# Optimization experiments

Hardware: AMD Instinct MI355X
Metric: run time of the kernel (lower is better)

## Reference

```python
import jax, jax.numpy as jnp
import numpy as np

N_NODES, N_EDGES, D_IN, N_GRAPHS = 20000, 320000, 256, 32
H1, C1, H2, C2 = 4, 128, 4, 64


def setup_inputs() -> dict:
    key = jax.random.key(0)
    ks = jax.random.split(key, 24)
    g = lambda k, shape, fan: jax.random.normal(k, shape, jnp.float32) * (1.0 / np.sqrt(fan))
    inp = {
        'x': jax.random.normal(ks[0], (N_NODES, D_IN), jnp.float32),
        'edge_index': jax.random.randint(ks[1], (2, N_EDGES), 0, N_NODES, jnp.int32),
        'batch': jnp.sort(jax.random.randint(ks[2], (N_NODES,), 0, N_GRAPHS, jnp.int32)),
        'edge_attr': jax.random.normal(ks[3], (N_EDGES, 1), jnp.float32),
        # GATConv 1: lin [D_IN, H1*C1], att_src/dst/edge [H1,C1], lin_edge [1,H1*C1], bias [H1*C1]
        'W1': g(ks[4], (D_IN, H1 * C1), D_IN),
        'as1': g(ks[5], (H1, C1), C1),
        'ad1': g(ks[6], (H1, C1), C1),
        'We1': g(ks[7], (1, H1 * C1), 1),
        'ae1': g(ks[8], (H1, C1), C1),
        'b1': jnp.zeros((H1 * C1,), jnp.float32),
        'g1': jnp.ones((H1 * C1,), jnp.float32),
        'be1': jnp.zeros((H1 * C1,), jnp.float32),
        # GATConv 2 (concat=False -> out 64)
        'W2': g(ks[9], (H1 * C1, H2 * C2), H1 * C1),
        'as2': g(ks[10], (H2, C2), C2),
        'ad2': g(ks[11], (H2, C2), C2),
        'We2': g(ks[12], (1, H2 * C2), 1),
        'ae2': g(ks[13], (H2, C2), C2),
        'b2': jnp.zeros((C2,), jnp.float32),
        'g2': jnp.ones((C2,), jnp.float32),
        'be2': jnp.zeros((C2,), jnp.float32),
        'fw1': g(ks[14], (C2, 32), C2),
        'fb1': jnp.zeros((32,), jnp.float32),
        'fw2': g(ks[15], (32, 1), 32),
        'fb2': jnp.zeros((1,), jnp.float32),
    }
    return inp


def _gat(x, src, dst, ea, W, a_s, a_d, We, a_e, bias, H, C, concat, n):
    h = (x @ W).reshape(n, H, C)                         # [N,H,C]
    al_s = jnp.einsum('nhc,hc->nh', h, a_s)              # [N,H]
    al_d = jnp.einsum('nhc,hc->nh', h, a_d)
    e = (ea @ We).reshape(-1, H, C)                      # [E',H,C]
    al_e = jnp.einsum('ehc,hc->eh', e, a_e)
    logits = jax.nn.leaky_relu(al_s[src] + al_d[dst] + al_e, 0.2)  # [E',H]
    m = jax.ops.segment_max(logits, dst, num_segments=n)
    m = jnp.where(jnp.isfinite(m), m, 0.0)
    p = jnp.exp(logits - m[dst])
    denom = jax.ops.segment_sum(p, dst, num_segments=n)
    alpha = p / (denom[dst] + 1e-16)                     # segment softmax
    out = jax.ops.segment_sum(h[src] * alpha[:, :, None], dst, num_segments=n)
    out = out.reshape(n, H * C) if concat else out.mean(axis=1)
    return out + bias


def _bn(x, gamma, beta):
    mu = x.mean(axis=0)
    var = x.var(axis=0)
    return gamma * (x - mu) * jax.lax.rsqrt(var + 1e-5) + beta


def reference(x, edge_index, batch, edge_attr, W1, as1, ad1, We1, ae1, b1, g1, be1,
              W2, as2, ad2, We2, ae2, b2, g2, be2, fw1, fb1, fw2, fb2):
    n = x.shape[0]
    loop = jnp.arange(n, dtype=edge_index.dtype)
    src = jnp.concatenate([edge_index[0], loop])
    dst = jnp.concatenate([edge_index[1], loop])
    # self-loop edge_attr filled with mean (PyG fill_value='mean')
    ea = jnp.concatenate([edge_attr, jnp.broadcast_to(edge_attr.mean(axis=0), (n, edge_attr.shape[1]))])

    h = _gat(x, src, dst, ea, W1, as1, ad1, We1, ae1, b1, H1, C1, True, n)
    h = jax.nn.elu(_bn(h, g1, be1))
    h = _gat(h, src, dst, ea, W2, as2, ad2, We2, ae2, b2, H2, C2, False, n)
    h = jax.nn.elu(_bn(h, g2, be2))

    sums = jax.ops.segment_sum(h, batch, num_segments=N_GRAPHS)
    cnt = jax.ops.segment_sum(jnp.ones((n,), h.dtype), batch, num_segments=N_GRAPHS)
    pooled = sums / jnp.maximum(cnt, 1.0)[:, None]       # global_mean_pool
    # dropout is identity in eval mode
    out = jax.nn.elu(pooled @ fw1 + fb1) @ fw2 + fb2
    return out
```

## Files before the change

### kernel.cpp

```cpp
#include <hip/hip_runtime.h>
#include <hip/hip_bf16.h>

#define N_NODES  20000
#define MPAD     20096
#define N_EDGES  320000
#define N_EP     (N_EDGES + N_NODES)
#define D_IN     256
#define N_GRAPHS 32
#define HH1 4
#define CC1 128
#define HH2 4
#define CC2 64
#define MAXDEG   128

#define XB_OFF      0ull
#define HB1_OFF     10289152ull
#define AGG1_OFF    30867456ull
#define HB2_OFF     51445760ull
#define OUT2_OFF    61734912ull
#define EAF_OFF     66854912ull
#define W1BT_OFF    68134912ull
#define W2BT_OFF    68397056ull
#define CSR_OFF     68659200ull
#define ROWPTR_OFF  71379200ull
#define GSTART_OFF  71459264ull
#define SMALL_OFF   71459520ull
#define SBUF_OFF    71485120ull
#define EAP_OFF     71485184ull
#define ALSP_OFF    71486464ull
#define ALDP_OFF    72129536ull
#define PMU1_OFF    72772608ull
#define PM21_OFF    73296896ull
#define PMU2_OFF    73821184ull
#define PM22_OFF    73886720ull
#define A1_OFF      73952256ull
#define B1_OFF      73954304ull
#define A2_OFF      73956352ull
#define B2_OFF      73956608ull
#define EAACC_OFF   73956864ull
#define ALS_OFF     73956928ull
#define ALD_OFF     74278464ull
#define DEG_OFF     74600000ull
#define CURS_OFF    74680000ull
#define FLAGZ_OFF   74760000ull
#define ZERO0_START DEG_OFF
#define ZERO0_SIZE  160128ull
#define PP_OFF      74760128ull

#define S_AS1 0
#define S_AD1 512
#define S_WE1 1024
#define S_AE1 1536
#define S_G1  2048
#define S_BE1 2560
#define S_AS2 3072
#define S_AD2 3328
#define S_WE2 3584
#define S_AE2 3840
#define S_G2  4096
#define S_BE2 4160
#define S_FW1 4224
#define S_FB1 6272
#define S_FW2 6304
#define S_FB2 6336

typedef __attribute__((ext_vector_type(8))) short bf8_t;
typedef __attribute__((ext_vector_type(4))) float f4_t;

__global__ void detect_dtype(const unsigned short* __restrict__ xr, int* __restrict__ flag) {
    int i = blockIdx.x * blockDim.x + threadIdx.x;
    unsigned short u = xr[i];
    if ((u & 0x7F80) == 0x7F80) atomicOr(flag, 1);
}

__device__ __forceinline__ float loadF(const void* p, int i, int fp32) {
    return fp32 ? ((const float*)p)[i]
                : __bfloat162float(((const __hip_bfloat16*)p)[i]);
}

#define PB_XB  5024
#define PB_EAF 313
#define PB_W   512
#define PB_SM  16
#define PREP_BLOCKS (PB_XB + PB_EAF + 2 * PB_W + PB_SM + 1)
__global__ __launch_bounds__(256) void prep(
        const int* __restrict__ flag,
        const void* x, const void* ea, const void* W1, const void* W2,
        const void* as1, const void* ad1, const void* We1, const void* ae1,
        const void* g1, const void* be1, const void* as2, const void* ad2,
        const void* We2, const void* ae2, const void* g2, const void* be2,
        const void* fw1, const void* fb1, const void* fw2, const void* fb2,
        __hip_bfloat16* __restrict__ xb, float* __restrict__ eaf, float* __restrict__ eap,
        __hip_bfloat16* __restrict__ W1bt, __hip_bfloat16* __restrict__ W2bt,
        float* __restrict__ smalls, float* __restrict__ sbuf) {
    __shared__ float sh[256];
    int b = blockIdx.x, t = threadIdx.x;
    int fp32 = flag[0];
    if (b < PB_XB) {
        int base = (b * 256 + t) * 4;
        __hip_bfloat16 tmp[4];
#pragma unroll
        for (int j = 0; j < 4; ++j) {
            int i = base + j;
            float v = (i < N_NODES * D_IN) ? loadF(x, i, fp32) : 0.f;
            tmp[j] = __float2bfloat16(v);
        }
        *(uint2*)&xb[base] = *(uint2*)tmp;
        return;
    }
    b -= PB_XB;
    if (b < PB_EAF) {
        int base = (b * 256 + t) * 4;
        float s = 0.f;
#pragma unroll
        for (int j = 0; j < 4; ++j) {
            int i = base + j;
            if (i < N_EDGES) { float v = loadF(ea, i, fp32); eaf[i] = v; s += v; }
        }
        sh[t] = s;
        __syncthreads();
        for (int st = 128; st; st >>= 1) {
            if (t < st) sh[t] += sh[t + st];
            __syncthreads();
        }
        if (t == 0) eap[b] = sh[0];
        return;
    }
    b -= PB_EAF;
    if (b < PB_W) {
        int i = b * 256 + t;
        int k = i >> 9, n = i & 511;
        W1bt[(size_t)n * 256 + k] = __float2bfloat16(loadF(W1, i, fp32));
        return;
    }
    b -= PB_W;
    if (b < PB_W) {
        int i = b * 256 + t;
        int k = i >> 8, n = i & 255;
        W2bt[(size_t)n * 512 + k] = __float2bfloat16(loadF(W2, i, fp32));
        return;
    }
    b -= PB_W;
    if (b < PB_SM) {
        const void* srcs[16] = {as1, ad1, We1, ae1, g1, be1, as2, ad2, We2, ae2, g2, be2, fw1, fb1, fw2, fb2};
        const int cnts[16] = {512, 512, 512, 512, 512, 512, 256, 256, 256, 256, 64, 64, 2048, 32, 32, 1};
        const int offs[16] = {S_AS1, S_AD1, S_WE1, S_AE1, S_G1, S_BE1, S_AS2, S_AD2,
                              S_WE2, S_AE2, S_G2, S_BE2, S_FW1, S_FB1, S_FW2, S_FB2};
        for (int i = t; i < cnts[b]; i += 256)
            smalls[offs[b] + i] = loadF(srcs[b], i, fp32);
        return;
    }
    if (t < 4) {
        float s = 0.f;
        for (int c = 0; c < CC1; ++c) s += loadF(We1, t * CC1 + c, fp32) * loadF(ae1, t * CC1 + c, fp32);
        sbuf[t] = s;
    } else if (t < 8) {
        int h = t - 4;
        float s = 0.f;
        for (int c = 0; c < CC2; ++c) s += loadF(We2, h * CC2 + c, fp32) * loadF(ae2, h * CC2 + c, fp32);
        sbuf[4 + h] = s;
    }
}

#define HIST_BLOCKS 1329
__global__ void hist_bounds(const int* __restrict__ ei, int* __restrict__ deg,
                            const int* __restrict__ batch, int* __restrict__ gstart) {
    int b = blockIdx.x, t = threadIdx.x;
    if (b < HIST_BLOCKS) {
        int e = b * 256 + t;
        if (e >= N_EP) return;
        int d = (e < N_EDGES) ? ei[N_EDGES + e] : e - N_EDGES;
        atomicAdd(&deg[d], 1);
        return;
    }
    int i = (b - HIST_BLOCKS) * 256 + t;
    if (i >= N_NODES) return;
    int bb = batch[i];
    if (i == 0) {
        for (int g = 0; g <= bb; ++g) gstart[g] = 0;
    } else {
        int pb = batch[i - 1];
        for (int g = pb + 1; g <= bb; ++g) gstart[g] = i;
    }
    if (i == N_NODES - 1) {
        for (int g = bb + 1; g <= N_GRAPHS; ++g) gstart[g] = N_NODES;
    }
}

__global__ __launch_bounds__(1024) void deg_scan(const int* __restrict__ deg, int* __restrict__ rowptr,
                                                 const float* __restrict__ eap, float* __restrict__ ea_acc) {
    __shared__ int part[1024];
    int t = threadIdx.x;
    int lo = t * 20;
    int hi = lo + 20; if (hi > N_NODES) hi = N_NODES; if (lo > N_NODES) lo = N_NODES;
    int s = 0;
    for (int i = lo; i < hi; ++i) s += deg[i];
    part[t] = s;
    __syncthreads();
    for (int off = 1; off < 1024; off <<= 1) {
        int u = (t >= off) ? part[t - off] : 0;
        __syncthreads();
        if (t >= off) part[t] += u;
        __syncthreads();
    }
    int run = part[t] - s;
    for (int i = lo; i < hi; ++i) { rowptr[i] = run; run += deg[i]; }
    if (hi == N_NODES && lo < N_NODES) rowptr[N_NODES] = run;
    if (t == 0) {
        float es = 0.f;
        for (int i = 0; i < PB_EAF; ++i) es += eap[i];
        ea_acc[0] = es;
    }
}

__global__ void edge_scatter(const int* __restrict__ ei, const int* __restrict__ rowptr,
                             int* __restrict__ cursor, int2* __restrict__ csr_se) {
    int e = blockIdx.x * blockDim.x + threadIdx.x;
    if (e >= N_EP) return;
    int s, d;
    if (e < N_EDGES) { s = ei[e]; d = ei[N_EDGES + e]; }
    else { s = d = e - N_EDGES; }
    int pos = rowptr[d] + atomicAdd(&cursor[d], 1);
    csr_se[pos] = make_int2(s, e);
}

__global__ __launch_bounds__(64) void csr_sort_fill(const int* __restrict__ rowptr, int2* __restrict__ cs,
                                                    const float* __restrict__ eaf,
                                                    const float* __restrict__ ea_acc) {
    __shared__ int2 buf[128];
    int d = blockIdx.x;
    int beg = rowptr[d], end = rowptr[d + 1], n = end - beg;
    int lane = threadIdx.x;
    float ea_mean = ea_acc[0] * (1.0f / N_EDGES);
    if (n <= 0) return;
    if (n <= 128) {
        for (int i = lane; i < n; i += 64) buf[i] = cs[beg + i];
        __syncthreads();
        for (int r = 0; r < n; ++r) {
            int i = 2 * lane + (r & 1);
            if (i + 1 < n) {
                int2 a = buf[i], b = buf[i + 1];
                if (a.y > b.y) { buf[i] = b; buf[i + 1] = a; }
            }
            __syncthreads();
        }
        for (int i = lane; i < n; i += 64) {
            int2 se = buf[i];
            float eav = (se.y < N_EDGES) ? eaf[se.y] : ea_mean;
            se.y = __float_as_int(eav);
            cs[beg + i] = se;
        }
    } else {
        if (lane == 0) {
            for (int i = beg + 1; i < end; ++i) {
                int2 key = cs[i]; int j = i - 1;
                while (j >= beg && cs[j].y > key.y) { cs[j + 1] = cs[j]; --j; }
                cs[j + 1] = key;
            }
        }
        __syncthreads();
        for (int i = lane; i < n; i += 64) {
            int2 se = cs[beg + i];
            float eav = (se.y < N_EDGES) ? eaf[se.y] : ea_mean;
            se.y = __float_as_int(eav);
            cs[beg + i] = se;
        }
    }
}

__global__ __launch_bounds__(256) void gemm_mfma_al(
        const short* __restrict__ A, const short* __restrict__ Bt,
        __hip_bfloat16* __restrict__ Cb, int N, int K,
        float* __restrict__ alsp, float* __restrict__ aldp,
        const float* __restrict__ asv, const float* __restrict__ adv, int cshift) {
    __shared__ short As[128 * 40];
    __shared__ short Bs[64 * 40];
    int t = threadIdx.x;
    int wv = t >> 6, lane = t & 63, quad = lane >> 4, lr = lane & 15;
    int m0 = blockIdx.y * 128, n0 = blockIdx.x * 64;
    f4_t acc[2][4] = {};
    int ra0 = t >> 2, sa0 = t & 3;
    int ra1 = (t + 256) >> 2;
    for (int k0 = 0; k0 < K; k0 += 32) {
        *(uint4*)&As[ra0 * 40 + sa0 * 8] = *(const uint4*)&A[(size_t)(m0 + ra0) * K + k0 + sa0 * 8];
        *(uint4*)&As[ra1 * 40 + sa0 * 8] = *(const uint4*)&A[(size_t)(m0 + ra1) * K + k0 + sa0 * 8];
        *(uint4*)&Bs[ra0 * 40 + sa0 * 8] = *(const uint4*)&Bt[(size_t)(n0 + ra0) * K + k0 + sa0 * 8];
        __syncthreads();
        bf8_t a0 = *(const bf8_t*)&As[(wv * 16 + lr) * 40 + quad * 8];
        bf8_t a1 = *(const bf8_t*)&As[((wv + 4) * 16 + lr) * 40 + quad * 8];
#pragma unroll
        for (int nt = 0; nt < 4; ++nt) {
            bf8_t b = *(const bf8_t*)&Bs[(nt * 16 + lr) * 40 + quad * 8];
            acc[0][nt] = __builtin_amdgcn_mfma_f32_16x16x32_bf16(a0, b, acc[0][nt], 0, 0, 0);
            acc[1][nt] = __builtin_amdgcn_mfma_f32_16x16x32_bf16(a1, b, acc[1][nt], 0, 0, 0);
        }
        __syncthreads();
    }
#pragma unroll
    for (int si = 0; si < 2; ++si) {
        int mrow = m0 + (wv + si * 4) * 16 + quad * 4;
#pragma unroll
        for (int nt = 0; nt < 4; ++nt) {
            int col = n0 + nt * 16 + lr;
#pragma unroll
            for (int r = 0; r < 4; ++r)
                Cb[(size_t)(mrow + r) * N + col] = __float2bfloat16(acc[si][nt][r]);
        }
    }
    float asv4[4], adv4[4];
#pragma unroll
    for (int nt = 0; nt < 4; ++nt) {
        asv4[nt] = asv[n0 + nt * 16 + lr];
        adv4[nt] = adv[n0 + nt * 16 + lr];
    }
    int hsel = n0 >> cshift;
    int parity = (n0 >> 6) & ((1 << (cshift - 6)) - 1);
#pragma unroll
    for (int si = 0; si < 2; ++si) {
#pragma unroll
        for (int r = 0; r < 4; ++r) {
            float ps = 0.f, pd = 0.f;
#pragma unroll
            for (int nt = 0; nt < 4; ++nt) {
                ps += acc[si][nt][r] * asv4[nt];
                pd += acc[si][nt][r] * adv4[nt];
            }
#pragma unroll
            for (int m = 1; m < 16; m <<= 1) {
                ps += __shfl_xor(ps, m);
                pd += __shfl_xor(pd, m);
            }
            if (lr == 0) {
                int row = m0 + (wv + si * 4) * 16 + quad * 4 + r;
                alsp[(row * 4 + hsel) * 2 + parity] = ps;
                aldp[(row * 4 + hsel) * 2 + parity] = pd;
            }
        }
    }
}

__global__ void al_combine(const float* __restrict__ alsp, const float* __restrict__ aldp,
                           float* __restrict__ als, float* __restrict__ ald, int nparts) {
    int i = blockIdx.x * blockDim.x + threadIdx.x;
    if (i >= MPAD * 4) return;
    float s = alsp[2 * i], d0 = aldp[2 * i];
    if (nparts == 2) { s += alsp[2 * i + 1]; d0 += aldp[2 * i + 1]; }
    als[i] = s; ald[i] = d0;
}

__global__ __launch_bounds__(128) void fused_agg1(
        const int* __restrict__ rowptr, const int2* __restrict__ cs,
        const float* __restrict__ als, const float* __restrict__ ald,
        const float* __restrict__ sbuf, const __hip_bfloat16* __restrict__ hb,
        __hip_bfloat16* __restrict__ outb) {
    __shared__ float lg[MAXDEG * 4];
    __shared__ int   ssrc[MAXDEG];
    __shared__ float red[4 * 128];
    __shared__ float mxs[4], dns[4];
    int d = blockIdx.x, t = threadIdx.x;
    int beg = rowptr[d], end = rowptr[d + 1], n = end - beg;
    bool fit = (n <= MAXDEG);
    float4 adv = *(const float4*)&ald[d * 4];
    float adh[4] = {adv.x, adv.y, adv.z, adv.w};
    float sb[4] = {sbuf[0], sbuf[1], sbuf[2], sbuf[3]};
    float mx[4] = {-INFINITY, -INFINITY, -INFINITY, -INFINITY};
    for (int p = t; p < n; p += 128) {
        int2 se = cs[beg + p];
        float eav = __int_as_float(se.y);
        float4 as = *(const float4*)&als[se.x * 4];
        float as4[4] = {as.x, as.y, as.z, as.w};
#pragma unroll
        for (int h = 0; h < 4; ++h) {
            float l = as4[h] + adh[h] + eav * sb[h];
            l = l > 0.f ? l : 0.2f * l;
            if (fit) lg[p * 4 + h] = l;
            mx[h] = fmaxf(mx[h], l);
        }
        if (fit) ssrc[p] = se.x;
    }
#pragma unroll
    for (int i = 0; i < 4; ++i) red[i * 128 + t] = mx[i];
    __syncthreads();
    for (int s = 64; s; s >>= 1) {
        if (t < s) {
#pragma unroll
            for (int i = 0; i < 4; ++i)
                red[i * 128 + t] = fmaxf(red[i * 128 + t], red[i * 128 + t + s]);
        }
        __syncthreads();
    }
    if (t < 4) mxs[t] = red[t * 128];
    __syncthreads();
    float m4[4] = {mxs[0], mxs[1], mxs[2], mxs[3]};
    float sm[4] = {0.f, 0.f, 0.f, 0.f};
    if (fit) {
        for (int p = t; p < n; p += 128) {
            float4 lv = *(float4*)&lg[p * 4];
            lv.x = __expf(lv.x - m4[0]); lv.y = __expf(lv.y - m4[1]);
            lv.z = __expf(lv.z - m4[2]); lv.w = __expf(lv.w - m4[3]);
            *(float4*)&lg[p * 4] = lv;
            sm[0] += lv.x; sm[1] += lv.y; sm[2] += lv.z; sm[3] += lv.w;
        }
    } else {
        for (int p = t; p < n; p += 128) {
            int2 se = cs[beg + p];
            float eav = __int_as_float(se.y);
            float4 as = *(const float4*)&als[se.x * 4];
            float as4[4] = {as.x, as.y, as.z, as.w};
#pragma unroll
            for (int h = 0; h < 4; ++h) {
                float l = as4[h] + adh[h] + eav * sb[h];
                l = l > 0.f ? l : 0.2f * l;
                sm[h] += __expf(l - m4[h]);
            }
        }
    }
    __syncthreads();
#pragma unroll
    for (int i = 0; i < 4; ++i) red[i * 128 + t] = sm[i];
    __syncthreads();
    for (int s = 64; s; s >>= 1) {
        if (t < s) {
#pragma unroll
            for (int i = 0; i < 4; ++i)
                red[i * 128 + t] += red[i * 128 + t + s];
        }
        __syncthreads();
    }
    if (t < 4) dns[t] = red[t * 128];
    __syncthreads();
    int h = t >> 5;
    float rdn = 1.0f / (dns[h] + 1e-16f);
    float a0 = 0.f, a1 = 0.f, a2 = 0.f, a3 = 0.f;
    if (fit) {
        for (int p = 0; p < n; ++p) {
            float w = lg[p * 4 + h];
            uint2 raw = *(const uint2*)&hb[(size_t)ssrc[p] * 512 + 4 * t];
            a0 += w * __uint_as_float(raw.x << 16);
            a1 += w * __uint_as_float(raw.x & 0xFFFF0000u);
            a2 += w * __uint_as_float(raw.y << 16);
            a3 += w * __uint_as_float(raw.y & 0xFFFF0000u);
        }
    } else {
        for (int p = 0; p < n; ++p) {
            int2 se = cs[beg + p];
            float eav = __int_as_float(se.y);
            float l = als[se.x * 4 + h] + adh[h] + eav * sb[h];
            l = l > 0.f ? l : 0.2f * l;
            float w = __expf(l - m4[h]);
            uint2 raw = *(const uint2*)&hb[(size_t)se.x * 512 + 4 * t];
            a0 += w * __uint_as_float(raw.x << 16);
            a1 += w * __uint_as_float(raw.x & 0xFFFF0000u);
            a2 += w * __uint_as_float(raw.y << 16);
            a3 += w * __uint_as_float(raw.y & 0xFFFF0000u);
        }
    }
    __hip_bfloat16 tmp[4] = {__float2bfloat16(a0 * rdn), __float2bfloat16(a1 * rdn),
                             __float2bfloat16(a2 * rdn), __float2bfloat16(a3 * rdn)};
    *(uint2*)&outb[(size_t)d * 512 + 4 * t] = *(uint2*)tmp;
}

__global__ __launch_bounds__(64) void fused_agg2(
        const int* __restrict__ rowptr, const int2* __restrict__ cs,
        const float* __restrict__ als, const float* __restrict__ ald,
        const float* __restrict__ sbuf, const __hip_bfloat16* __restrict__ hb,
        float* __restrict__ out2) {
    __shared__ float lg[MAXDEG * 4];
    __shared__ int   ssrc[MAXDEG];
    __shared__ float red[4 * 64];
    __shared__ float mxs[4], dns[4];
    __shared__ float shm[256];
    int d = blockIdx.x, t = threadIdx.x;
    int beg = rowptr[d], end = rowptr[d + 1], n = end - beg;
    bool fit = (n <= MAXDEG);
    float4 adv = *(const float4*)&ald[d * 4];
    float adh[4] = {adv.x, adv.y, adv.z, adv.w};
    float sb[4] = {sbuf[4], sbuf[5], sbuf[6], sbuf[7]};
    float mx[4] = {-INFINITY, -INFINITY, -INFINITY, -INFINITY};
    for (int p = t; p < n; p += 64) {
        int2 se = cs[beg + p];
        float eav = __int_as_float(se.y);
        float4 as = *(const float4*)&als[se.x * 4];
        float as4[4] = {as.x, as.y, as.z, as.w};
#pragma unroll
        for (int h = 0; h < 4; ++h) {
            float l = as4[h] + adh[h] + eav * sb[h];
            l = l > 0.f ? l : 0.2f * l;
            if (fit) lg[p * 4 + h] = l;
            mx[h] = fmaxf(mx[h], l);
        }
        if (fit) ssrc[p] = se.x;
    }
#pragma unroll
    for (int i = 0; i < 4; ++i) red[i * 64 + t] = mx[i];
    __syncthreads();
    for (int s = 32; s; s >>= 1) {
        if (t < s) {
#pragma unroll
            for (int i = 0; i < 4; ++i)
                red[i * 64 + t] = fmaxf(red[i * 64 + t], red[i * 64 + t + s]);
        }
        __syncthreads();
    }
    if (t < 4) mxs[t] = red[t * 64];
    __syncthreads();
    float m4[4] = {mxs[0], mxs[1], mxs[2], mxs[3]};
    float sm[4] = {0.f, 0.f, 0.f, 0.f};
    if (fit) {
        for (int p = t; p < n; p += 64) {
            float4 lv = *(float4*)&lg[p * 4];
            lv.x = __expf(lv.x - m4[0]); lv.y = __expf(lv.y - m4[1]);
            lv.z = __expf(lv.z - m4[2]); lv.w = __expf(lv.w - m4[3]);
            *(float4*)&lg[p * 4] = lv;
            sm[0] += lv.x; sm[1] += lv.y; sm[2] += lv.z; sm[3] += lv.w;
        }
    } else {
        for (int p = t; p < n; p += 64) {
            int2 se = cs[beg + p];
            float eav = __int_as_float(se.y);
            float4 as = *(const float4*)&als[se.x * 4];
            float as4[4] = {as.x, as.y, as.z, as.w};
#pragma unroll
            for (int h = 0; h < 4; ++h) {
                float l = as4[h] + adh[h] + eav * sb[h];
                l = l > 0.f ? l : 0.2f * l;
                sm[h] += __expf(l - m4[h]);
            }
        }
    }
    __syncthreads();
#pragma unroll
    for (int i = 0; i < 4; ++i) red[i * 64 + t] = sm[i];
    __syncthreads();
    for (int s = 32; s; s >>= 1) {
        if (t < s) {
#pragma unroll
            for (int i = 0; i < 4; ++i)
                red[i * 64 + t] += red[i * 64 + t + s];
        }
        __syncthreads();
    }
    if (t < 4) dns[t] = red[t * 64];
    __syncthreads();
    int h = t >> 4;
    float rdn = 1.0f / (dns[h] + 1e-16f);
    float a0 = 0.f, a1 = 0.f, a2 = 0.f, a3 = 0.f;
    if (fit) {
        for (int p = 0; p < n; ++p) {
            float w = lg[p * 4 + h];
            uint2 raw = *(const uint2*)&hb[(size_t)ssrc[p] * 256 + 4 * t];
            a0 += w * __uint_as_float(raw.x << 16);
            a1 += w * __uint_as_float(raw.x & 0xFFFF0000u);
            a2 += w * __uint_as_float(raw.y << 16);
            a3 += w * __uint_as_float(raw.y & 0xFFFF0000u);
        }
    } else {
        for (int p = 0; p < n; ++p) {
            int2 se = cs[beg + p];
            float eav = __int_as_float(se.y);
            float l = als[se.x * 4 + h] + adh[h] + eav * sb[h];
            l = l > 0.f ? l : 0.2f * l;
            float w = __expf(l - m4[h]);
            uint2 raw = *(const uint2*)&hb[(size_t)se.x * 256 + 4 * t];
            a0 += w * __uint_as_float(raw.x << 16);
            a1 += w * __uint_as_float(raw.x & 0xFFFF0000u);
            a2 += w * __uint_as_float(raw.y << 16);
            a3 += w * __uint_as_float(raw.y & 0xFFFF0000u);
        }
    }
    shm[4 * t] = a0 * rdn; shm[4 * t + 1] = a1 * rdn;
    shm[4 * t + 2] = a2 * rdn; shm[4 * t + 3] = a3 * rdn;
    __syncthreads();
    if (t < 16) {
        float4 v;
        v.x = 0.25f * (shm[4 * t] + shm[64 + 4 * t] + shm[128 + 4 * t] + shm[192 + 4 * t]);
        v.y = 0.25f * (shm[4 * t + 1] + shm[64 + 4 * t + 1] + shm[128 + 4 * t + 1] + shm[192 + 4 * t + 1]);
        v.z = 0.25f * (shm[4 * t + 2] + shm[64 + 4 * t + 2] + shm[128 + 4 * t + 2] + shm[192 + 4 * t + 2]);
        v.w = 0.25f * (shm[4 * t + 3] + shm[64 + 4 * t + 3] + shm[128 + 4 * t + 3] + shm[192 + 4 * t + 3]);
        *(float4*)&out2[(size_t)d * 64 + 4 * t] = v;
    }
}

__global__ __launch_bounds__(256) void bn_part_b(const __hip_bfloat16* __restrict__ x,
                                                 float* __restrict__ pmu, float* __restrict__ pm2) {
    int t = threadIdx.x, b = blockIdx.x;
    float s0 = 0.f, s20 = 0.f, s1 = 0.f, s21 = 0.f;
    for (int i = b; i < N_NODES; i += gridDim.x) {
        unsigned u = *(const unsigned*)&x[(size_t)i * 512 + 2 * t];
        float v0 = __uint_as_float(u << 16);
        float v1 = __uint_as_float(u & 0xFFFF0000u);
        s0 += v0; s20 += v0 * v0; s1 += v1; s21 += v1 * v1;
    }
    pmu[b * 512 + 2 * t] = s0;     pm2[b * 512 + 2 * t] = s20;
    pmu[b * 512 + 2 * t + 1] = s1; pm2[b * 512 + 2 * t + 1] = s21;
}

__global__ void bn_reduce_affine(const float* __restrict__ pmu, const float* __restrict__ pm2,
                                 const float* __restrict__ smalls, int s_g, int s_be,
                                 float* __restrict__ a, float* __restrict__ b, int nch) {
    int c = blockIdx.x * blockDim.x + threadIdx.x;
    if (c >= nch) return;
    float s = 0.f, s2 = 0.f;
    for (int bk = 0; bk < 256; ++bk) { s += pmu[bk * nch + c]; s2 += pm2[bk * nch + c]; }
    float m = s * (1.0f / N_NODES);
    float var = s2 * (1.0f / N_NODES) - m * m;
    float aa = smalls[s_g + c] * rsqrtf(var + 1e-5f);
    a[c] = aa;
    b[c] = smalls[s_be + c] - m * aa;
}

__global__ __launch_bounds__(256) void bn_apply_elu_b16(__hip_bfloat16* __restrict__ x,
                                                        const float* __restrict__ a,
                                                        const float* __restrict__ b) {
    int q = blockIdx.x * blockDim.x + threadIdx.x;
    if (q >= N_NODES * 512 / 4) return;
    int base = q * 4;
    int j = base & 511;
    uint2 raw = *(uint2*)&x[base];
    float v[4] = {__uint_as_float(raw.x << 16), __uint_as_float(raw.x & 0xFFFF0000u),
                  __uint_as_float(raw.y << 16), __uint_as_float(raw.y & 0xFFFF0000u)};
    __hip_bfloat16 tmp[4];
#pragma unroll
    for (int k = 0; k < 4; ++k) {
        float y = a[j + k] * v[k] + b[j + k];
        y = y > 0.f ? y : expm1f(y);
        tmp[k] = __float2bfloat16(y);
    }
    *(uint2*)&x[base] = *(uint2*)tmp;
}

__global__ __launch_bounds__(256) void bn2_stats(const float* __restrict__ x,
                                                 float* __restrict__ pmu, float* __restrict__ pm2) {
    int t = threadIdx.x;
    int c = t & 63, j = t >> 6;
    float ls = 0.f, ls2 = 0.f;
    for (int nd = blockIdx.x * 4 + j; nd < N_NODES; nd += gridDim.x * 4) {
        float v = x[(size_t)nd * 64 + c];
        ls += v; ls2 += v * v;
    }
    __shared__ float shs[4][64], sh2[4][64];
    shs[j][c] = ls; sh2[j][c] = ls2;
    __syncthreads();
    if (j == 0) {
        pmu[blockIdx.x * 64 + c] = shs[0][c] + shs[1][c] + shs[2][c] + shs[3][c];
        pm2[blockIdx.x * 64 + c] = sh2[0][c] + sh2[1][c] + sh2[2][c] + sh2[3][c];
    }
}

__global__ __launch_bounds__(256) void pool_part(const float* __restrict__ x, const int* __restrict__ gstart,
                                                 const float* __restrict__ a2, const float* __restrict__ b2,
                                                 float* __restrict__ pp) {
    int g = blockIdx.x >> 3, ck = blockIdx.x & 7;
    int t = threadIdx.x;
    int c = t & 63, j = t >> 6;
    int beg = gstart[g], end = gstart[g + 1], n = end - beg;
    int cb = beg + (n * ck) / 8, ce = beg + (n * (ck + 1)) / 8;
    float ac = a2[c], bc = b2[c];
    float s = 0.f;
    for (int i = cb + j; i < ce; i += 4) {
        float y = ac * x[(size_t)i * 64 + c] + bc;
        s += (y > 0.f ? y : expm1f(y));
    }
    __shared__ float sh[4][64];
    sh[j][c] = s;
    __syncthreads();
    if (j == 0)
        pp[blockIdx.x * 64 + c] = sh[0][c] + sh[1][c] + sh[2][c] + sh[3][c];
}

__global__ __launch_bounds__(64) void pool_mlp_fin(const float* __restrict__ pp, const int* __restrict__ gstart,
                                                   const float* __restrict__ smalls, const int* __restrict__ flag,
                                                   void* __restrict__ outp) {
    int g = blockIdx.x, t = threadIdx.x;
    __shared__ float pooled[64];
    __shared__ float hsh[32];
    float s = 0.f;
    for (int k = 0; k < 8; ++k) s += pp[(g * 8 + k) * 64 + t];
    int n = gstart[g + 1] - gstart[g];
    pooled[t] = s / fmaxf((float)n, 1.0f);
    __syncthreads();
    if (t < 32) {
        float acc = smalls[S_FB1 + t];
        for (int cc = 0; cc < 64; ++cc)
            acc += pooled[cc] * smalls[S_FW1 + cc * 32 + t];
        hsh[t] = acc > 0.f ? acc : expm1f(acc);
    }
    __syncthreads();
    if (t == 0) {
        float o = smalls[S_FB2];
        for (int k = 0; k < 32; ++k) o += hsh[k] * smalls[S_FW2 + k];
        if (flag[0]) ((float*)outp)[g] = o;
        else ((__hip_bfloat16*)outp)[g] = __float2bfloat16(o);
    }
}

extern "C" void kernel_launch(void* const* d_in, const int* in_sizes, int n_in,
                              void* d_out, int out_size, void* d_ws, size_t ws_size,
                              hipStream_t stream) {
    const void* x    = d_in[0];
    const int* ei    = (const int*)d_in[1];
    const int* batch = (const int*)d_in[2];
    const void* ea   = d_in[3];
    const void* W1   = d_in[4];
    const void* as1  = d_in[5];
    const void* ad1  = d_in[6];
    const void* We1  = d_in[7];
    const void* ae1  = d_in[8];
    const void* g1   = d_in[10];
    const void* be1  = d_in[11];
    const void* W2   = d_in[12];
    const void* as2  = d_in[13];
    const void* ad2  = d_in[14];
    const void* We2  = d_in[15];
    const void* ae2  = d_in[16];
    const void* g2   = d_in[18];
    const void* be2  = d_in[19];
    const void* fw1  = d_in[20];
    const void* fb1  = d_in[21];
    const void* fw2  = d_in[22];
    const void* fb2  = d_in[23];

    char* ws = (char*)d_ws;
    __hip_bfloat16* xb   = (__hip_bfloat16*)(ws + XB_OFF);
    __hip_bfloat16* hb1  = (__hip_bfloat16*)(ws + HB1_OFF);
    __hip_bfloat16* agg1 = (__hip_bfloat16*)(ws + AGG1_OFF);
    __hip_bfloat16* hb2  = (__hip_bfloat16*)(ws + HB2_OFF);
    float* out2   = (float*)(ws + OUT2_OFF);
    float* eaf    = (float*)(ws + EAF_OFF);
    __hip_bfloat16* W1bt = (__hip_bfloat16*)(ws + W1BT_OFF);
    __hip_bfloat16* W2bt = (__hip_bfloat16*)(ws + W2BT_OFF);
    int2*  csr_se = (int2*)(ws + CSR_OFF);
    int*   rowptr = (int*)(ws + ROWPTR_OFF);
    int*   gstart = (int*)(ws + GSTART_OFF);
    float* smalls = (float*)(ws + SMALL_OFF);
    float* sbuf   = (float*)(ws + SBUF_OFF);
    float* eap    = (float*)(ws + EAP_OFF);
    float* alsp   = (float*)(ws + ALSP_OFF);
    float* aldp   = (float*)(ws + ALDP_OFF);
    float* pmu1   = (float*)(ws + PMU1_OFF);
    float* pm21   = (float*)(ws + PM21_OFF);
    float* pmu2   = (float*)(ws + PMU2_OFF);
    float* pm22   = (float*)(ws + PM22_OFF);
    float* a1     = (float*)(ws + A1_OFF);
    float* b1     = (float*)(ws + B1_OFF);
    float* a2     = (float*)(ws + A2_OFF);
    float* b2     = (float*)(ws + B2_OFF);
    float* ea_acc = (float*)(ws + EAACC_OFF);
    float* als    = (float*)(ws + ALS_OFF);
    float* ald    = (float*)(ws + ALD_OFF);
    float* pp     = (float*)(ws + PP_OFF);
    int*   deg    = (int*)(ws + DEG_OFF);
    int*   cursor = (int*)(ws + CURS_OFF);
    int*   flag   = (int*)(ws + FLAGZ_OFF);

    hipMemsetAsync(ws + ZERO0_START, 0, ZERO0_SIZE, stream);

    detect_dtype<<<256, 256, 0, stream>>>((const unsigned short*)x, flag);
    prep<<<PREP_BLOCKS, 256, 0, stream>>>(flag, x, ea, W1, W2,
                                          as1, ad1, We1, ae1, g1, be1, as2, ad2,
                                          We2, ae2, g2, be2, fw1, fb1, fw2, fb2,
                                          xb, eaf, eap, W1bt, W2bt, smalls, sbuf);

    hist_bounds<<<HIST_BLOCKS + 79, 256, 0, stream>>>(ei, deg, batch, gstart);
    deg_scan<<<1, 1024, 0, stream>>>(deg, rowptr, eap, ea_acc);
    edge_scatter<<<HIST_BLOCKS, 256, 0, stream>>>(ei, rowptr, cursor, csr_se);
    csr_sort_fill<<<N_NODES, 64, 0, stream>>>(rowptr, csr_se, eaf, ea_acc);

    gemm_mfma_al<<<dim3(512 / 64, MPAD / 128), 256, 0, stream>>>(
        (const short*)xb, (const short*)W1bt, hb1, 512, 256,
        alsp, aldp, smalls + S_AS1, smalls + S_AD1, 7);
    al_combine<<<(MPAD * 4 + 255) / 256, 256, 0, stream>>>(alsp, aldp, als, ald, 2);
    fused_agg1<<<N_NODES, 128, 0, stream>>>(rowptr, csr_se, als, ald, sbuf, hb1, agg1);
    bn_part_b<<<256, 256, 0, stream>>>(agg1, pmu1, pm21);
    bn_reduce_affine<<<2, 256, 0, stream>>>(pmu1, pm21, smalls, S_G1, S_BE1, a1, b1, 512);
    bn_apply_elu_b16<<<10000, 256, 0, stream>>>(agg1, a1, b1);

    gemm_mfma_al<<<dim3(256 / 64, MPAD / 128), 256, 0, stream>>>(
        (const short*)agg1, (const short*)W2bt, hb2, 256, 512,
        alsp, aldp, smalls + S_AS2, smalls + S_AD2, 6);
    al_combine<<<(MPAD * 4 + 255) / 256, 256, 0, stream>>>(alsp, aldp, als, ald, 1);
    fused_agg2<<<N_NODES, 64, 0, stream>>>(rowptr, csr_se, als, ald, sbuf, hb2, out2);
    bn2_stats<<<256, 256, 0, stream>>>(out2, pmu2, pm22);
    bn_reduce_affine<<<1, 64, 0, stream>>>(pmu2, pm22, smalls, S_G2, S_BE2, a2, b2, 64);

    pool_part<<<N_GRAPHS * 8, 256, 0, stream>>>(out2, gstart, a2, b2, pp);
    pool_mlp_fin<<<N_GRAPHS, 64, 0, stream>>>(pp, gstart, smalls, flag, d_out);
}
```

Before: 425.1 us.

## Use one wavefront per destination node in GAT aggregation kernels

Both aggregation kernels now give each 64-lane wavefront its own destination node, two nodes per block. Block-wide shared-memory reductions with many __syncthreads are replaced by wave shuffles. The softmax exp and denominator are folded into the gather loop, which is unrolled by four to keep more loads in flight. Layer 1 uses 16-byte loads with 8 channels per lane. The aim is to cut synchronization, reduction overhead and launch count, but each lane carries more registers and the per-head max is now reduced over the whole wave.

```diff
diff --git a/kernel.cpp b/kernel.cpp
--- a/kernel.cpp
+++ b/kernel.cpp
@@ -353,232 +353,184 @@
         const float* __restrict__ als, const float* __restrict__ ald,
         const float* __restrict__ sbuf, const __hip_bfloat16* __restrict__ hb,
         __hip_bfloat16* __restrict__ outb) {
-    __shared__ float lg[MAXDEG * 4];
-    __shared__ int   ssrc[MAXDEG];
-    __shared__ float red[4 * 128];
-    __shared__ float mxs[4], dns[4];
-    int d = blockIdx.x, t = threadIdx.x;
-    int beg = rowptr[d], end = rowptr[d + 1], n = end - beg;
+    __shared__ float lg[2][MAXDEG * 4];
+    __shared__ int   ssrc[2][MAXDEG];
+    int wv = threadIdx.x >> 6, t = threadIdx.x & 63;
+    int d = blockIdx.x * 2 + wv;
+    int beg = rowptr[d], n = rowptr[d + 1] - beg;
     bool fit = (n <= MAXDEG);
     float4 adv = *(const float4*)&ald[d * 4];
     float adh[4] = {adv.x, adv.y, adv.z, adv.w};
-    float sb[4] = {sbuf[0], sbuf[1], sbuf[2], sbuf[3]};
-    float mx[4] = {-INFINITY, -INFINITY, -INFINITY, -INFINITY};
-    for (int p = t; p < n; p += 128) {
-        int2 se = cs[beg + p];
-        float eav = __int_as_float(se.y);
-        float4 as = *(const float4*)&als[se.x * 4];
-        float as4[4] = {as.x, as.y, as.z, as.w};
-#pragma unroll
-        for (int h = 0; h < 4; ++h) {
-            float l = as4[h] + adh[h] + eav * sb[h];
-            l = l > 0.f ? l : 0.2f * l;
-            if (fit) lg[p * 4 + h] = l;
-            mx[h] = fmaxf(mx[h], l);
-        }
-        if (fit) ssrc[p] = se.x;
-    }
-#pragma unroll
-    for (int i = 0; i < 4; ++i) red[i * 128 + t] = mx[i];
-    __syncthreads();
-    for (int s = 64; s; s >>= 1) {
-        if (t < s) {
-#pragma unroll
-            for (int i = 0; i < 4; ++i)
-                red[i * 128 + t] = fmaxf(red[i * 128 + t], red[i * 128 + t + s]);
-        }
-        __syncthreads();
-    }
-    if (t < 4) mxs[t] = red[t * 128];
-    __syncthreads();
-    float m4[4] = {mxs[0], mxs[1], mxs[2], mxs[3]};
-    float sm[4] = {0.f, 0.f, 0.f, 0.f};
-    if (fit) {
-        for (int p = t; p < n; p += 128) {
-            float4 lv = *(float4*)&lg[p * 4];
-            lv.x = __expf(lv.x - m4[0]); lv.y = __expf(lv.y - m4[1]);
-            lv.z = __expf(lv.z - m4[2]); lv.w = __expf(lv.w - m4[3]);
-            *(float4*)&lg[p * 4] = lv;
-            sm[0] += lv.x; sm[1] += lv.y; sm[2] += lv.z; sm[3] += lv.w;
-        }
-    } else {
-        for (int p = t; p < n; p += 128) {
-            int2 se = cs[beg + p];
-            float eav = __int_as_float(se.y);
-            float4 as = *(const float4*)&als[se.x * 4];
-            float as4[4] = {as.x, as.y, as.z, as.w};
-#pragma unroll
-            for (int h = 0; h < 4; ++h) {
-                float l = as4[h] + adh[h] + eav * sb[h];
-                l = l > 0.f ? l : 0.2f * l;
-                sm[h] += __expf(l - m4[h]);
-            }
-        }
-    }
-    __syncthreads();
-#pragma unroll
-    for (int i = 0; i < 4; ++i) red[i * 128 + t] = sm[i];
-    __syncthreads();
-    for (int s = 64; s; s >>= 1) {
-        if (t < s) {
-#pragma unroll
-            for (int i = 0; i < 4; ++i)
-                red[i * 128 + t] += red[i * 128 + t + s];
-        }
-        __syncthreads();
-    }
-    if (t < 4) dns[t] = red[t * 128];
-    __syncthreads();
-    int h = t >> 5;
-    float rdn = 1.0f / (dns[h] + 1e-16f);
-    float a0 = 0.f, a1 = 0.f, a2 = 0.f, a3 = 0.f;
-    if (fit) {
-        for (int p = 0; p < n; ++p) {
-            float w = lg[p * 4 + h];
-            uint2 raw = *(const uint2*)&hb[(size_t)ssrc[p] * 512 + 4 * t];
-            a0 += w * __uint_as_float(raw.x << 16);
-            a1 += w * __uint_as_float(raw.x & 0xFFFF0000u);
-            a2 += w * __uint_as_float(raw.y << 16);
-            a3 += w * __uint_as_float(raw.y & 0xFFFF0000u);
-        }
-    } else {
-        for (int p = 0; p < n; ++p) {
-            int2 se = cs[beg + p];
-            float eav = __int_as_float(se.y);
-            float l = als[se.x * 4 + h] + adh[h] + eav * sb[h];
-            l = l > 0.f ? l : 0.2f * l;
-            float w = __expf(l - m4[h]);
-            uint2 raw = *(const uint2*)&hb[(size_t)se.x * 512 + 4 * t];
-            a0 += w * __uint_as_float(raw.x << 16);
-            a1 += w * __uint_as_float(raw.x & 0xFFFF0000u);
-            a2 += w * __uint_as_float(raw.y << 16);
-            a3 += w * __uint_as_float(raw.y & 0xFFFF0000u);
-        }
-    }
-    __hip_bfloat16 tmp[4] = {__float2bfloat16(a0 * rdn), __float2bfloat16(a1 * rdn),
-                             __float2bfloat16(a2 * rdn), __float2bfloat16(a3 * rdn)};
-    *(uint2*)&outb[(size_t)d * 512 + 4 * t] = *(uint2*)tmp;
-}
-
-__global__ __launch_bounds__(64) void fused_agg2(
-        const int* __restrict__ rowptr, const int2* __restrict__ cs,
-        const float* __restrict__ als, const float* __restrict__ ald,
-        const float* __restrict__ sbuf, const __hip_bfloat16* __restrict__ hb,
-        float* __restrict__ out2) {
-    __shared__ float lg[MAXDEG * 4];
-    __shared__ int   ssrc[MAXDEG];
-    __shared__ float red[4 * 64];
-    __shared__ float mxs[4], dns[4];
-    __shared__ float shm[256];
-    int d = blockIdx.x, t = threadIdx.x;
-    int beg = rowptr[d], end = rowptr[d + 1], n = end - beg;
-    bool fit = (n <= MAXDEG);
-    float4 adv = *(const float4*)&ald[d * 4];
-    float adh[4] = {adv.x, adv.y, adv.z, adv.w};
-    float sb[4] = {sbuf[4], sbuf[5], sbuf[6], sbuf[7]};
+    float sb4[4] = {sbuf[0], sbuf[1], sbuf[2], sbuf[3]};
     float mx[4] = {-INFINITY, -INFINITY, -INFINITY, -INFINITY};
     for (int p = t; p < n; p += 64) {
         int2 se = cs[beg + p];
         float eav = __int_as_float(se.y);
         float4 as = *(const float4*)&als[se.x * 4];
-        float as4[4] = {as.x, as.y, as.z, as.w};
-#pragma unroll
-        for (int h = 0; h < 4; ++h) {
-            float l = as4[h] + adh[h] + eav * sb[h];
-            l = l > 0.f ? l : 0.2f * l;
-            if (fit) lg[p * 4 + h] = l;
-            mx[h] = fmaxf(mx[h], l);
-        }
-        if (fit) ssrc[p] = se.x;
-    }
-#pragma unroll
-    for (int i = 0; i < 4; ++i) red[i * 64 + t] = mx[i];
-    __syncthreads();
-    for (int s = 32; s; s >>= 1) {
-        if (t < s) {
-#pragma unroll
-            for (int i = 0; i < 4; ++i)
-                red[i * 64 + t] = fmaxf(red[i * 64 + t], red[i * 64 + t + s]);
-        }
-        __syncthreads();
-    }
-    if (t < 4) mxs[t] = red[t * 64];
-    __syncthreads();
-    float m4[4] = {mxs[0], mxs[1], mxs[2], mxs[3]};
-    float sm[4] = {0.f, 0.f, 0.f, 0.f};
-    if (fit) {
-        for (int p = t; p < n; p += 64) {
-            float4 lv = *(float4*)&lg[p * 4];
-            lv.x = __expf(lv.x - m4[0]); lv.y = __expf(lv.y - m4[1]);
-            lv.z = __expf(lv.z - m4[2]); lv.w = __expf(lv.w - m4[3]);
-            *(float4*)&lg[p * 4] = lv;
-            sm[0] += lv.x; sm[1] += lv.y; sm[2] += lv.z; sm[3] += lv.w;
-        }
-    } else {
-        for (int p = t; p < n; p += 64) {
-            int2 se = cs[beg + p];
-            float eav = __int_as_float(se.y);
-            float4 as = *(const float4*)&als[se.x * 4];
-            float as4[4] = {as.x, as.y, as.z, as.w};
-#pragma unroll
-            for (int h = 0; h < 4; ++h) {
-                float l = as4[h] + adh[h] + eav * sb[h];
-                l = l > 0.f ? l : 0.2f * l;
-                sm[h] += __expf(l - m4[h]);
-            }
-        }
-    }
-    __syncthreads();
-#pragma unroll
-    for (int i = 0; i < 4; ++i) red[i * 64 + t] = sm[i];
-    __syncthreads();
-    for (int s = 32; s; s >>= 1) {
-        if (t < s) {
-#pragma unroll
-            for (int i = 0; i < 4; ++i)
-                red[i * 64 + t] += red[i * 64 + t + s];
-        }
-        __syncthreads();
-    }
-    if (t < 4) dns[t] = red[t * 64];
+        float l[4] = {as.x, as.y, as.z, as.w};
+#pragma unroll
+        for (int hh = 0; hh < 4; ++hh) {
+            float v = l[hh] + adh[hh] + eav * sb4[hh];
+            v = v > 0.f ? v : 0.2f * v;
+            l[hh] = v;
+            mx[hh] = fmaxf(mx[hh], v);
+        }
+        if (fit) {
+            *(float4*)&lg[wv][p * 4] = make_float4(l[0], l[1], l[2], l[3]);
+            ssrc[wv][p] = se.x;
+        }
+    }
+#pragma unroll
+    for (int m = 1; m < 64; m <<= 1)
+#pragma unroll
+        for (int hh = 0; hh < 4; ++hh)
+            mx[hh] = fmaxf(mx[hh], __shfl_xor(mx[hh], m));
     __syncthreads();
     int h = t >> 4;
-    float rdn = 1.0f / (dns[h] + 1e-16f);
-    float a0 = 0.f, a1 = 0.f, a2 = 0.f, a3 = 0.f;
+    float mh = mx[h];
+    float a[8] = {};
+    float ds = 0.f;
+    const __hip_bfloat16* hrow = hb + 8 * t;
+#define ACC8(rr, wt) { \
+    unsigned q0 = (rr).x, q1 = (rr).y, q2 = (rr).z, q3 = (rr).w; \
+    a[0] += (wt) * __uint_as_float(q0 << 16); a[1] += (wt) * __uint_as_float(q0 & 0xFFFF0000u); \
+    a[2] += (wt) * __uint_as_float(q1 << 16); a[3] += (wt) * __uint_as_float(q1 & 0xFFFF0000u); \
+    a[4] += (wt) * __uint_as_float(q2 << 16); a[5] += (wt) * __uint_as_float(q2 & 0xFFFF0000u); \
+    a[6] += (wt) * __uint_as_float(q3 << 16); a[7] += (wt) * __uint_as_float(q3 & 0xFFFF0000u); }
     if (fit) {
-        for (int p = 0; p < n; ++p) {
-            float w = lg[p * 4 + h];
-            uint2 raw = *(const uint2*)&hb[(size_t)ssrc[p] * 256 + 4 * t];
-            a0 += w * __uint_as_float(raw.x << 16);
-            a1 += w * __uint_as_float(raw.x & 0xFFFF0000u);
-            a2 += w * __uint_as_float(raw.y << 16);
-            a3 += w * __uint_as_float(raw.y & 0xFFFF0000u);
+        int p = 0;
+        for (; p + 4 <= n; p += 4) {
+            int s0 = ssrc[wv][p], s1 = ssrc[wv][p + 1], s2 = ssrc[wv][p + 2], s3 = ssrc[wv][p + 3];
+            uint4 r0 = *(const uint4*)&hrow[(size_t)s0 * 512];
+            uint4 r1 = *(const uint4*)&hrow[(size_t)s1 * 512];
+            uint4 r2 = *(const uint4*)&hrow[(size_t)s2 * 512];
+            uint4 r3 = *(const uint4*)&hrow[(size_t)s3 * 512];
+            float w0 = __expf(lg[wv][p * 4 + h] - mh);
+            float w1 = __expf(lg[wv][p * 4 + 4 + h] - mh);
+            float w2 = __expf(lg[wv][p * 4 + 8 + h] - mh);
+            float w3 = __expf(lg[wv][p * 4 + 12 + h] - mh);
+            ds += (w0 + w1) + (w2 + w3);
+            ACC8(r0, w0); ACC8(r1, w1); ACC8(r2, w2); ACC8(r3, w3);
+        }
+        for (; p < n; ++p) {
+            int s0 = ssrc[wv][p];
+            uint4 r0 = *(const uint4*)&hrow[(size_t)s0 * 512];
+            float w0 = __expf(lg[wv][p * 4 + h] - mh);
+            ds += w0;
+            ACC8(r0, w0);
         }
     } else {
         for (int p = 0; p < n; ++p) {
             int2 se = cs[beg + p];
             float eav = __int_as_float(se.y);
-            float l = als[se.x * 4 + h] + adh[h] + eav * sb[h];
+            float l = als[se.x * 4 + h] + adh[h] + eav * sb4[h];
             l = l > 0.f ? l : 0.2f * l;
-            float w = __expf(l - m4[h]);
-            uint2 raw = *(const uint2*)&hb[(size_t)se.x * 256 + 4 * t];
-            a0 += w * __uint_as_float(raw.x << 16);
-            a1 += w * __uint_as_float(raw.x & 0xFFFF0000u);
-            a2 += w * __uint_as_float(raw.y << 16);
-            a3 += w * __uint_as_float(raw.y & 0xFFFF0000u);
-        }
-    }
-    shm[4 * t] = a0 * rdn; shm[4 * t + 1] = a1 * rdn;
-    shm[4 * t + 2] = a2 * rdn; shm[4 * t + 3] = a3 * rdn;
+            float w = __expf(l - mh);
+            uint4 r0 = *(const uint4*)&hrow[(size_t)se.x * 512];
+            ds += w;
+            ACC8(r0, w);
+        }
+    }
+#undef ACC8
+    float rdn = 1.0f / (ds + 1e-16f);
+    __hip_bfloat16 tmp[8];
+#pragma unroll
+    for (int j = 0; j < 8; ++j) tmp[j] = __float2bfloat16(a[j] * rdn);
+    *(uint4*)&outb[(size_t)d * 512 + 8 * t] = *(uint4*)tmp;
+}
+
+__global__ __launch_bounds__(128) void fused_agg2(
+        const int* __restrict__ rowptr, const int2* __restrict__ cs,
+        const float* __restrict__ als, const float* __restrict__ ald,
+        const float* __restrict__ sbuf, const __hip_bfloat16* __restrict__ hb,
+        float* __restrict__ out2) {
+    __shared__ float lg[2][MAXDEG * 4];
+    __shared__ int   ssrc[2][MAXDEG];
+    int wv = threadIdx.x >> 6, t = threadIdx.x & 63;
+    int d = blockIdx.x * 2 + wv;
+    int beg = rowptr[d], n = rowptr[d + 1] - beg;
+    bool fit = (n <= MAXDEG);
+    float4 adv = *(const float4*)&ald[d * 4];
+    float adh[4] = {adv.x, adv.y, adv.z, adv.w};
+    float sb4[4] = {sbuf[4], sbuf[5], sbuf[6], sbuf[7]};
+    float mx[4] = {-INFINITY, -INFINITY, -INFINITY, -INFINITY};
+    for (int p = t; p < n; p += 64) {
+        int2 se = cs[beg + p];
+        float eav = __int_as_float(se.y);
+        float4 as = *(const float4*)&als[se.x * 4];
+        float l[4] = {as.x, as.y, as.z, as.w};
+#pragma unroll
+        for (int hh = 0; hh < 4; ++hh) {
+            float v = l[hh] + adh[hh] + eav * sb4[hh];
+            v = v > 0.f ? v : 0.2f * v;
+            l[hh] = v;
+            mx[hh] = fmaxf(mx[hh], v);
+        }
+        if (fit) {
+            *(float4*)&lg[wv][p * 4] = make_float4(l[0], l[1], l[2], l[3]);
+            ssrc[wv][p] = se.x;
+        }
+    }
+#pragma unroll
+    for (int m = 1; m < 64; m <<= 1)
+#pragma unroll
+        for (int hh = 0; hh < 4; ++hh)
+            mx[hh] = fmaxf(mx[hh], __shfl_xor(mx[hh], m));
     __syncthreads();
-    if (t < 16) {
-        float4 v;
-        v.x = 0.25f * (shm[4 * t] + shm[64 + 4 * t] + shm[128 + 4 * t] + shm[192 + 4 * t]);
-        v.y = 0.25f * (shm[4 * t + 1] + shm[64 + 4 * t + 1] + shm[128 + 4 * t + 1] + shm[192 + 4 * t + 1]);
-        v.z = 0.25f * (shm[4 * t + 2] + shm[64 + 4 * t + 2] + shm[128 + 4 * t + 2] + shm[192 + 4 * t + 2]);
-        v.w = 0.25f * (shm[4 * t + 3] + shm[64 + 4 * t + 3] + shm[128 + 4 * t + 3] + shm[192 + 4 * t + 3]);
-        *(float4*)&out2[(size_t)d * 64 + 4 * t] = v;
-    }
+    int h = t >> 4;
+    float mh = mx[h];
+    float a4[4] = {};
+    float ds = 0.f;
+    const __hip_bfloat16* hrow = hb + 4 * t;
+#define ACC4(rr, wt) { \
+    unsigned q0 = (rr).x, q1 = (rr).y; \
+    a4[0] += (wt) * __uint_as_float(q0 << 16); a4[1] += (wt) * __uint_as_float(q0 & 0xFFFF0000u); \
+    a4[2] += (wt) * __uint_as_float(q1 << 16); a4[3] += (wt) * __uint_as_float(q1 & 0xFFFF0000u); }
+    if (fit) {
+        int p = 0;
+        for (; p + 4 <= n; p += 4) {
+            int s0 = ssrc[wv][p], s1 = ssrc[wv][p + 1], s2 = ssrc[wv][p + 2], s3 = ssrc[wv][p + 3];
+            uint2 r0 = *(const uint2*)&hrow[(size_t)s0 * 256];
+            uint2 r1 = *(const uint2*)&hrow[(size_t)s1 * 256];
+            uint2 r2 = *(const uint2*)&hrow[(size_t)s2 * 256];
+            uint2 r3 = *(const uint2*)&hrow[(size_t)s3 * 256];
+            float w0 = __expf(lg[wv][p * 4 + h] - mh);
+            float w1 = __expf(lg[wv][p * 4 + 4 + h] - mh);
+            float w2 = __expf(lg[wv][p * 4 + 8 + h] - mh);
+            float w3 = __expf(lg[wv][p * 4 + 12 + h] - mh);
+            ds += (w0 + w1) + (w2 + w3);
+            ACC4(r0, w0); ACC4(r1, w1); ACC4(r2, w2); ACC4(r3, w3);
+        }
+        for (; p < n; ++p) {
+            int s0 = ssrc[wv][p];
+            uint2 r0 = *(const uint2*)&hrow[(size_t)s0 * 256];
+            float w0 = __expf(lg[wv][p * 4 + h] - mh);
+            ds += w0;
+            ACC4(r0, w0);
+        }
+    } else {
+        for (int p = 0; p < n; ++p) {
+            int2 se = cs[beg + p];
+            float eav = __int_as_float(se.y);
+            float l = als[se.x * 4 + h] + adh[h] + eav * sb4[h];
+            l = l > 0.f ? l : 0.2f * l;
+            float w = __expf(l - mh);
+            uint2 r0 = *(const uint2*)&hrow[(size_t)se.x * 256];
+            ds += w;
+            ACC4(r0, w);
+        }
+    }
+#undef ACC4
+    float rdn = 1.0f / (ds + 1e-16f);
+#pragma unroll
+    for (int j = 0; j < 4; ++j) {
+        float v = a4[j] * rdn;
+        v += __shfl_xor(v, 16);
+        v += __shfl_xor(v, 32);
+        a4[j] = v * 0.25f;
+    }
+    if (t < 16)
+        *(float4*)&out2[(size_t)d * 64 + 4 * t] = make_float4(a4[0], a4[1], a4[2], a4[3]);
 }
 
 __global__ __launch_bounds__(256) void bn_part_b(const __hip_bfloat16* __restrict__ x,
@@ -770,7 +722,7 @@
         (const short*)xb, (const short*)W1bt, hb1, 512, 256,
         alsp, aldp, smalls + S_AS1, smalls + S_AD1, 7);
     al_combine<<<(MPAD * 4 + 255) / 256, 256, 0, stream>>>(alsp, aldp, als, ald, 2);
-    fused_agg1<<<N_NODES, 128, 0, stream>>>(rowptr, csr_se, als, ald, sbuf, hb1, agg1);
+    fused_agg1<<<N_NODES / 2, 128, 0, stream>>>(rowptr, csr_se, als, ald, sbuf, hb1, agg1);
     bn_part_b<<<256, 256, 0, stream>>>(agg1, pmu1, pm21);
     bn_reduce_affine<<<2, 256, 0, stream>>>(pmu1, pm21, smalls, S_G1, S_BE1, a1, b1, 512);
     bn_apply_elu_b16<<<10000, 256, 0, stream>>>(agg1, a1, b1);
@@ -779,7 +731,7 @@
         (const short*)agg1, (const short*)W2bt, hb2, 256, 512,
         alsp, aldp, smalls + S_AS2, smalls + S_AD2, 6);
     al_combine<<<(MPAD * 4 + 255) / 256, 256, 0, stream>>>(alsp, aldp, als, ald, 1);
-    fused_agg2<<<N_NODES, 64, 0, stream>>>(rowptr, csr_se, als, ald, sbuf, hb2, out2);
+    fused_agg2<<<N_NODES / 2, 128, 0, stream>>>(rowptr, csr_se, als, ald, sbuf, hb2, out2);
     bn2_stats<<<256, 256, 0, stream>>>(out2, pmu2, pm22);
     bn_reduce_affine<<<1, 64, 0, stream>>>(pmu2, pm22, smalls, S_G2, S_BE2, a2, b2, 64);
 
```

After: 422.3 us. No clear change (-0.6%).
